# Kernel optimization log

Measured on AMD Instinct MI355X. Metric: run time of the kernel, lower is better.

Reference implementation:

```python
import jax, jax.numpy as jnp
import numpy as np
import math

H, NH, DH, FF = 768, 12, 64, 3072
B, S = 8, 1024

def _gelu(x):
    return x * 0.5 * (1.0 + jax.lax.erf(x / math.sqrt(2.0)))

def _layernorm(x, gamma, beta, eps=1e-6):
    mean = jnp.mean(x, axis=-1, keepdims=True)
    std = jnp.std(x, axis=-1, keepdims=True, ddof=1)  # torch unbiased std
    return gamma * (x - mean) / (std + eps) + beta

def setup_inputs() -> dict:
    key = jax.random.key(0)
    ks = jax.random.split(key, 16)
    p = lambda k, shape: jax.random.normal(k, shape, dtype=jnp.float32) * 0.02
    return {
        "hidden": jax.random.normal(ks[0], (B, S, H), dtype=jnp.float32),
        "mask": jnp.zeros((B, 1, S, S), dtype=jnp.float32),
        "position_bias": jax.random.normal(ks[1], (1, NH, S, S), dtype=jnp.float32),
        "Wq": p(ks[2], (H, H)), "bq": jnp.zeros((H,), jnp.float32),
        "Wk": p(ks[3], (H, H)), "bk": jnp.zeros((H,), jnp.float32),
        "Wv": p(ks[4], (H, H)), "bv": jnp.zeros((H,), jnp.float32),
        "Wo": p(ks[5], (H, H)), "bo": jnp.zeros((H,), jnp.float32),
        "W1": p(ks[6], (H, FF)), "b1": jnp.zeros((FF,), jnp.float32),
        "W2": p(ks[7], (FF, H)), "b2": jnp.zeros((H,), jnp.float32),
        "g1": jnp.ones((H,), jnp.float32), "beta1": jnp.zeros((H,), jnp.float32),
        "g2": jnp.ones((H,), jnp.float32), "beta2": jnp.zeros((H,), jnp.float32),
    }

def reference(hidden, mask, position_bias, Wq, bq, Wk, bk, Wv, bv, Wo, bo,
              W1, b1, W2, b2, g1, beta1, g2, beta2):
    b, s, _ = hidden.shape
    def split_heads(x):
        return x.reshape(b, s, NH, DH).transpose(0, 2, 1, 3)  # [b, h, s, d]
    q = split_heads(hidden @ Wq + bq)
    k = split_heads(hidden @ Wk + bk)
    v = split_heads(hidden @ Wv + bv)
    scores = jnp.einsum('bhqd,bhkd->bhqk', q, k)
    scores = scores + position_bias          # bias added BEFORE scaling (as in source)
    scores = scores / math.sqrt(float(DH))
    scores = scores + mask
    probs = jax.nn.softmax(scores, axis=-1)  # dropout is identity in eval
    ctx = jnp.einsum('bhqk,bhkd->bhqd', probs, v)
    ctx = ctx.transpose(0, 2, 1, 3).reshape(b, s, NH * DH)
    attn_out = ctx @ Wo + bo
    inter = _layernorm(attn_out + hidden, g1, beta1)
    ffn = _gelu(inter @ W1 + b1) @ W2 + b2
    return _layernorm(ffn + inter, g2, beta2)
```

## Files before the change

### kernel.cpp

```cpp
#include <hip/hip_runtime.h>
#include <cmath>

typedef __bf16 bf16;
typedef __attribute__((ext_vector_type(8))) __bf16 bf16x8;
typedef __attribute__((ext_vector_type(4))) __bf16 bf16x4;
typedef __attribute__((ext_vector_type(4))) float f32x4;

#define DEVINL __device__ __forceinline__

DEVINL void gload16(const void* g, void* l) {
    __builtin_amdgcn_global_load_lds((const __attribute__((address_space(1))) void*)g,
                                     (__attribute__((address_space(3))) void*)l, 16, 0, 0);
}


__global__ void cast_bf16_kernel(const float* __restrict__ in, bf16* __restrict__ out, int n4) {
    int i = blockIdx.x * 256 + threadIdx.x;
    if (i < n4) {
        float4 v = ((const float4*)in)[i];
        bf16x4 o;
        o[0] = (bf16)v.x; o[1] = (bf16)v.y; o[2] = (bf16)v.z; o[3] = (bf16)v.w;
        ((bf16x4*)out)[i] = o;
    }
}

__global__ void scale_cast_kernel(const float* __restrict__ in, bf16* __restrict__ out,
                                  float scale, int n4) {
    int i = blockIdx.x * 256 + threadIdx.x;
    if (i < n4) {
        float4 v = ((const float4*)in)[i];
        bf16x4 o;
        o[0] = (bf16)(v.x * scale); o[1] = (bf16)(v.y * scale);
        o[2] = (bf16)(v.z * scale); o[3] = (bf16)(v.w * scale);
        ((bf16x4*)out)[i] = o;
    }
}

__global__ void tcast_kernel(const float* __restrict__ in, bf16* __restrict__ out, int R, int C) {
    __shared__ float t[32][33];
    int tx = threadIdx.x & 31, ty = threadIdx.x >> 5;
    int r0 = blockIdx.y * 32, c0 = blockIdx.x * 32;
#pragma unroll
    for (int i = 0; i < 4; ++i)
        t[ty + 8 * i][tx] = in[(size_t)(r0 + ty + 8 * i) * C + c0 + tx];
    __syncthreads();
#pragma unroll
    for (int i = 0; i < 4; ++i)
        out[(size_t)(c0 + ty + 8 * i) * R + r0 + tx] = (bf16)t[tx][ty + 8 * i];
}

__global__ void concat_bias_kernel(const float* __restrict__ a, const float* __restrict__ b,
                                   const float* __restrict__ c, float* __restrict__ out) {
    int i = blockIdx.x * 256 + threadIdx.x;
    if (i < 2304) out[i] = (i < 768) ? a[i] : ((i < 1536) ? b[i - 768] : c[i - 1536]);
}

__global__ __launch_bounds__(256) void vtrans_kernel(const bf16* __restrict__ qkv,
                                                     bf16* __restrict__ vT) {
    __shared__ bf16 t[64][72];
    const int tid = threadIdx.x;
    const int bh = blockIdx.y, s0 = blockIdx.x * 32;
    const int b = bh / 12, h = bh % 12;
    {
        const int r = tid >> 3, c8 = (tid & 7) * 8;
        bf16x8 v = *(const bf16x8*)(qkv + (size_t)(b * 1024 + s0 + r) * 2304 + 1536 + h * 64 + c8);
#pragma unroll
        for (int j = 0; j < 8; ++j) t[c8 + j][r] = v[j];
    }
    __syncthreads();
    {
        const int d = tid >> 2, s8 = (tid & 3) * 8;
        bf16x8 o = *(const bf16x8*)(&t[d][s8]);
        *(bf16x8*)(vT + (size_t)(bh * 64 + d) * 1024 + s0 + s8) = o;
    }
}

template<int MODE>
__global__ void gemm_kernel(const bf16* __restrict__ A, const bf16* __restrict__ Bt,
                            const float* __restrict__ bias,
                            bf16* __restrict__ Cb, float* __restrict__ Cf,
                            int M, int N, int K, int ldc) {
    __shared__ __align__(16) bf16 As[128 * 64];
    __shared__ __align__(16) bf16 Bs[128 * 64];
    const int tid = threadIdx.x;
    const int wid = tid >> 6, lane = tid & 63;
    const int L = blockIdx.y * gridDim.x + blockIdx.x;
    const int cpx = (gridDim.x * gridDim.y) >> 3;
    const int wg = (L & 7) * cpx + (L >> 3);
    const int m0 = (wg / gridDim.x) * 128, n0 = (wg % gridDim.x) * 128;
    const int wr = (wid >> 1) * 64, wc = (wid & 1) * 64;
    const int lg = lane >> 4, l15 = lane & 15;
    f32x4 acc[4][4] = {};

    for (int k0 = 0; k0 < K; k0 += 64) {
        __syncthreads();
#pragma unroll
        for (int i = 0; i < 4; ++i) {
            const int cbase = (wid * 4 + i) * 1024;
            const int td = cbase + lane * 16;
            const int row = td >> 7;
            const int s16 = ((td >> 4) & 7) ^ (row & 7);
            gload16(A + (size_t)(m0 + row) * K + k0 + s16 * 8, (char*)As + cbase);
            gload16(Bt + (size_t)(n0 + row) * K + k0 + s16 * 8, (char*)Bs + cbase);
        }
        __syncthreads();
#pragma unroll
        for (int kk = 0; kk < 2; ++kk) {
            bf16x8 af[4], bfr[4];
#pragma unroll
            for (int mi = 0; mi < 4; ++mi) {
                int ra = wr + mi * 16 + l15;
                int off = (ra * 128 + (kk * 32 + 8 * lg) * 2) ^ ((ra & 7) << 4);
                af[mi] = *(const bf16x8*)((const char*)As + off);
            }
#pragma unroll
            for (int ni = 0; ni < 4; ++ni) {
                int rb = wc + ni * 16 + l15;
                int off = (rb * 128 + (kk * 32 + 8 * lg) * 2) ^ ((rb & 7) << 4);
                bfr[ni] = *(const bf16x8*)((const char*)Bs + off);
            }
#pragma unroll
            for (int mi = 0; mi < 4; ++mi)
#pragma unroll
                for (int ni = 0; ni < 4; ++ni)
                    acc[mi][ni] = __builtin_amdgcn_mfma_f32_16x16x32_bf16(af[mi], bfr[ni], acc[mi][ni], 0, 0, 0);
        }
    }
#pragma unroll
    for (int mi = 0; mi < 4; ++mi) {
#pragma unroll
        for (int r = 0; r < 4; ++r) {
            const int row = m0 + wr + mi * 16 + lg * 4 + r;
#pragma unroll
            for (int ni = 0; ni < 4; ++ni) {
                const int col = n0 + wc + ni * 16 + l15;
                float v = acc[mi][ni][r] + bias[col];
                if (MODE == 2) v = v * 0.5f * (1.0f + erff(v * 0.70710678118654752f));
                if (MODE == 1) Cf[(size_t)row * ldc + col] = v;
                else           Cb[(size_t)row * ldc + col] = (bf16)v;
            }
        }
    }
}

__global__ __launch_bounds__(256, 3) void attn_kernel(const bf16* __restrict__ qkv,
                                                      const bf16* __restrict__ pbs,
                                                      const bf16* __restrict__ maskb,
                                                      const bf16* __restrict__ vT,
                                                      bf16* __restrict__ ctx) {
    __shared__ __align__(16) bf16 Kb[3][64 * 64];
    __shared__ __align__(16) bf16 Vb[3][64 * 64];
    const int tid = threadIdx.x, wid = tid >> 6, lane = tid & 63;
    const int bh = blockIdx.y, b = bh / 12, h = bh % 12;
    const int q0 = blockIdx.x * 128 + wid * 32;
    const int lg = lane >> 4, l15 = lane & 15;
    const float cqk = 0.18033688011112042f;

    bf16x8 aq[2][2];
#pragma unroll
    for (int qs = 0; qs < 2; ++qs) {
        const size_t r = (size_t)(b * 1024 + q0 + qs * 16 + l15) * 2304 + h * 64 + 8 * lg;
        aq[qs][0] = *(const bf16x8*)(qkv + r);
        aq[qs][1] = *(const bf16x8*)(qkv + r + 32);
    }

    auto stage = [&](int tt, int pp) {
#pragma unroll
        for (int rd = 0; rd < 2; ++rd) {
            const int n = rd * 256 + tid;
            const int i = n >> 3, sl = n & 7, c = sl ^ (i & 7);
            const int sig = (i & 32) | ((i & 12) << 1) | ((i & 16) >> 2) | (i & 3);
            gload16(qkv + (size_t)(b * 1024 + tt * 64 + sig) * 2304 + 768 + h * 64 + c * 8,
                    (char*)Kb[pp] + n * 16);
            gload16(vT + ((size_t)bh * 64 + i) * 1024 + tt * 64 + c * 8,
                    (char*)Vb[pp] + n * 16);
        }
    };

    float mrun[2] = {-1e30f, -1e30f}, lsum[2] = {0.f, 0.f};
    f32x4 acc[2][4] = {};

    stage(0, 0);
    stage(1, 1);
    __syncthreads();
    for (int t = 0; t < 16; ++t) {
        const int p = t % 3;
        const int k0 = t * 64;
        bf16x8 pbv[2][2], mkv[2][2];
#pragma unroll
        for (int qs = 0; qs < 2; ++qs) {
            const int q = q0 + qs * 16 + l15;
            const bf16* pr = pbs + ((size_t)h * 1024 + q) * 1024 + k0 + lg * 8;
            const bf16* mr = maskb + ((size_t)b * 1024 + q) * 1024 + k0 + lg * 8;
            pbv[qs][0] = *(const bf16x8*)pr;  pbv[qs][1] = *(const bf16x8*)(pr + 32);
            mkv[qs][0] = *(const bf16x8*)mr;  mkv[qs][1] = *(const bf16x8*)(mr + 32);
        }
        if (t < 14) stage(t + 2, (t + 2) % 3);

        bf16x8 bk[4][2];
#pragma unroll
        for (int kt = 0; kt < 4; ++kt) {
            const int row = kt * 16 + l15;
            const int byte = (row * 128 + lg * 16) ^ ((row & 7) << 4);
            bk[kt][0] = *(const bf16x8*)((const char*)Kb[p] + byte);
            bk[kt][1] = *(const bf16x8*)((const char*)Kb[p] + (byte ^ 64));
        }
        f32x4 s[2][4];
#pragma unroll
        for (int qs = 0; qs < 2; ++qs)
#pragma unroll
            for (int kt = 0; kt < 4; ++kt) {
                f32x4 z = {};
                z = __builtin_amdgcn_mfma_f32_16x16x32_bf16(bk[kt][0], aq[qs][0], z, 0, 0, 0);
                z = __builtin_amdgcn_mfma_f32_16x16x32_bf16(bk[kt][1], aq[qs][1], z, 0, 0, 0);
                s[qs][kt] = z;
            }
#pragma unroll
        for (int qs = 0; qs < 2; ++qs)
#pragma unroll
            for (int kt = 0; kt < 4; ++kt)
#pragma unroll
                for (int r = 0; r < 4; ++r) {
                    const int j = (kt & 1) * 4 + r;
                    s[qs][kt][r] = s[qs][kt][r] * cqk
                                 + (float)pbv[qs][kt >> 1][j]
                                 + (float)mkv[qs][kt >> 1][j];
                }
        bf16x8 po[2][2];
#pragma unroll
        for (int qs = 0; qs < 2; ++qs) {
            float tm = s[qs][0][0];
#pragma unroll
            for (int kt = 0; kt < 4; ++kt)
#pragma unroll
                for (int r = 0; r < 4; ++r) tm = fmaxf(tm, s[qs][kt][r]);
            tm = fmaxf(tm, __shfl_xor(tm, 16));
            tm = fmaxf(tm, __shfl_xor(tm, 32));
            const float mn = fmaxf(mrun[qs], tm);
            const float scal = __builtin_amdgcn_exp2f(mrun[qs] - mn);
            mrun[qs] = mn;
            float ts = 0.f;
#pragma unroll
            for (int kt = 0; kt < 4; ++kt)
#pragma unroll
                for (int r = 0; r < 4; ++r) {
                    const float pv = __builtin_amdgcn_exp2f(s[qs][kt][r] - mn);
                    ts += pv;
                    const int idx = kt * 4 + r;
                    if (idx < 8) po[qs][0][idx] = (bf16)pv;
                    else         po[qs][1][idx - 8] = (bf16)pv;
                }
            ts += __shfl_xor(ts, 16);
            ts += __shfl_xor(ts, 32);
            lsum[qs] = lsum[qs] * scal + ts;
#pragma unroll
            for (int dt = 0; dt < 4; ++dt) {
                acc[qs][dt][0] *= scal; acc[qs][dt][1] *= scal;
                acc[qs][dt][2] *= scal; acc[qs][dt][3] *= scal;
            }
        }
        bf16x8 vb[4][2];
#pragma unroll
        for (int dt = 0; dt < 4; ++dt) {
            const int row = dt * 16 + l15;
            const int byte = (row * 128 + lg * 16) ^ ((row & 7) << 4);
            vb[dt][0] = *(const bf16x8*)((const char*)Vb[p] + byte);
            vb[dt][1] = *(const bf16x8*)((const char*)Vb[p] + (byte ^ 64));
        }
#pragma unroll
        for (int qs = 0; qs < 2; ++qs)
#pragma unroll
            for (int dt = 0; dt < 4; ++dt) {
                acc[qs][dt] = __builtin_amdgcn_mfma_f32_16x16x32_bf16(vb[dt][0], po[qs][0], acc[qs][dt], 0, 0, 0);
                acc[qs][dt] = __builtin_amdgcn_mfma_f32_16x16x32_bf16(vb[dt][1], po[qs][1], acc[qs][dt], 0, 0, 0);
            }
        __syncthreads();
    }
    char* scr = (char*)Kb + wid * 4096;
#pragma unroll
    for (int qs = 0; qs < 2; ++qs) {
        const float inv = 1.0f / lsum[qs];
        const int ql = qs * 16 + l15;
#pragma unroll
        for (int dt = 0; dt < 4; ++dt) {
            bf16x4 o;
#pragma unroll
            for (int r = 0; r < 4; ++r) o[r] = (bf16)(acc[qs][dt][r] * inv);
            const int wb = (ql * 128 + dt * 32 + lg * 8) ^ ((ql & 7) << 4);
            *(bf16x4*)(scr + wb) = o;
        }
    }
    __syncthreads();
#pragma unroll
    for (int qs = 0; qs < 2; ++qs) {
        const int ql = qs * 16 + l15;
        const int rb = (ql * 128 + lg * 32) ^ ((ql & 7) << 4);
        bf16x8 o0 = *(const bf16x8*)(scr + rb);
        bf16x8 o1 = *(const bf16x8*)(scr + (rb ^ 16));
        bf16* cp = ctx + (size_t)(b * 1024 + q0 + ql) * 768 + h * 64 + lg * 16;
        *(bf16x8*)cp = o0;
        *(bf16x8*)(cp + 8) = o1;
    }
}

template<int MODE>
__global__ __launch_bounds__(256) void ln_kernel(const float* __restrict__ x, const float* __restrict__ res,
                                                 const float* __restrict__ g, const float* __restrict__ bt,
                                                 float* __restrict__ outf, bf16* __restrict__ outb) {
    const int wid = threadIdx.x >> 6, lane = threadIdx.x & 63;
    const int row = blockIdx.x * 4 + wid;
    const float4* xr = (const float4*)(x + (size_t)row * 768);
    const float4* rr = (const float4*)(res + (size_t)row * 768);
    float4 v[3];
    float s = 0.f, ss = 0.f;
#pragma unroll
    for (int j = 0; j < 3; ++j) {
        float4 a = xr[lane + 64 * j];
        float4 b = rr[lane + 64 * j];
        float4 w;
        w.x = a.x + b.x; w.y = a.y + b.y; w.z = a.z + b.z; w.w = a.w + b.w;
        v[j] = w;
        s += w.x + w.y + w.z + w.w;
        ss += w.x * w.x + w.y * w.y + w.z * w.z + w.w * w.w;
    }
#pragma unroll
    for (int off = 1; off <= 32; off <<= 1) { s += __shfl_xor(s, off); ss += __shfl_xor(ss, off); }
    const float mean = s * (1.f / 768.f);
    float var = (ss - 768.f * mean * mean) * (1.f / 767.f);
    var = fmaxf(var, 0.f);
    const float inv = 1.f / (sqrtf(var) + 1e-6f);
#pragma unroll
    for (int j = 0; j < 3; ++j) {
        float4 gv = ((const float4*)g)[lane + 64 * j];
        float4 bv = ((const float4*)bt)[lane + 64 * j];
        float4 y;
        y.x = gv.x * (v[j].x - mean) * inv + bv.x;
        y.y = gv.y * (v[j].y - mean) * inv + bv.y;
        y.z = gv.z * (v[j].z - mean) * inv + bv.z;
        y.w = gv.w * (v[j].w - mean) * inv + bv.w;
        ((float4*)(outf + (size_t)row * 768))[lane + 64 * j] = y;
        if (MODE == 0) {
            bf16x4 o;
            o[0] = (bf16)y.x; o[1] = (bf16)y.y; o[2] = (bf16)y.z; o[3] = (bf16)y.w;
            ((bf16x4*)(outb + (size_t)row * 768))[lane + 64 * j] = o;
        }
    }
}


extern "C" void kernel_launch(void* const* d_in, const int* in_sizes, int n_in,
                              void* d_out, int out_size, void* d_ws, size_t ws_size,
                              hipStream_t stream) {
    const float* hidden = (const float*)d_in[0];
    const float* mask   = (const float*)d_in[1];
    const float* pb     = (const float*)d_in[2];
    const float* Wq = (const float*)d_in[3];
    const float* bq = (const float*)d_in[4];
    const float* Wk = (const float*)d_in[5];
    const float* bk = (const float*)d_in[6];
    const float* Wv = (const float*)d_in[7];
    const float* bv = (const float*)d_in[8];
    const float* Wo = (const float*)d_in[9];
    const float* bo = (const float*)d_in[10];
    const float* W1 = (const float*)d_in[11];
    const float* b1 = (const float*)d_in[12];
    const float* W2 = (const float*)d_in[13];
    const float* b2 = (const float*)d_in[14];
    const float* g1  = (const float*)d_in[15];
    const float* be1 = (const float*)d_in[16];
    const float* g2  = (const float*)d_in[17];
    const float* be2 = (const float*)d_in[18];
    float* out = (float*)d_out;

    char* ws = (char*)d_ws;
    bf16*  xbf     = (bf16*)(ws);
    bf16*  wqkv_t  = (bf16*)(ws + 12582912);
    bf16*  wo_t    = (bf16*)(ws + 16121856);
    bf16*  w1_t    = (bf16*)(ws + 17301504);
    bf16*  w2_t    = (bf16*)(ws + 22020096);
    float* bqkv    = (float*)(ws + 26738688);
    bf16*  qkv     = (bf16*)(ws + 26747904);
    bf16*  ffn1    = qkv;
    bf16*  vT      = (bf16*)(ws + 26747904 + 37748736);
    bf16*  ctx     = (bf16*)(ws + 77079552);
    float* attn_out= (float*)(ws + 89662464);
    bf16*  pbs     = (bf16*)(ws + 89662464);
    float* ffn2    = attn_out;
    float* interf  = (float*)(ws + 114828288);
    bf16*  maskb   = (bf16*)(ws + 114828288);
    bf16*  interb  = xbf;

    const float log2e = 1.4426950408889634f;

    cast_bf16_kernel<<<6291456 / 4 / 256, 256, 0, stream>>>(hidden, xbf, 6291456 / 4);
    tcast_kernel<<<dim3(24, 24), 256, 0, stream>>>(Wq, wqkv_t, 768, 768);
    tcast_kernel<<<dim3(24, 24), 256, 0, stream>>>(Wk, wqkv_t + 768 * 768, 768, 768);
    tcast_kernel<<<dim3(24, 24), 256, 0, stream>>>(Wv, wqkv_t + 2 * 768 * 768, 768, 768);
    tcast_kernel<<<dim3(24, 24), 256, 0, stream>>>(Wo, wo_t, 768, 768);
    tcast_kernel<<<dim3(96, 24), 256, 0, stream>>>(W1, w1_t, 768, 3072);
    tcast_kernel<<<dim3(24, 96), 256, 0, stream>>>(W2, w2_t, 3072, 768);
    concat_bias_kernel<<<9, 256, 0, stream>>>(bq, bk, bv, bqkv);
    scale_cast_kernel<<<12582912 / 4 / 256, 256, 0, stream>>>(pb, pbs, 0.125f * log2e, 12582912 / 4);
    scale_cast_kernel<<<8388608 / 4 / 256, 256, 0, stream>>>(mask, maskb, log2e, 8388608 / 4);

    gemm_kernel<0><<<dim3(18, 64), 256, 0, stream>>>(xbf, wqkv_t, bqkv, qkv, nullptr, 8192, 2304, 768, 2304);
    vtrans_kernel<<<dim3(32, 96), 256, 0, stream>>>(qkv, vT);
    attn_kernel<<<dim3(8, 96), 256, 0, stream>>>(qkv, pbs, maskb, vT, ctx);
    gemm_kernel<1><<<dim3(6, 64), 256, 0, stream>>>(ctx, wo_t, bo, nullptr, attn_out, 8192, 768, 768, 768);
    ln_kernel<0><<<2048, 256, 0, stream>>>(attn_out, hidden, g1, be1, interf, interb);
    gemm_kernel<2><<<dim3(24, 64), 256, 0, stream>>>(interb, w1_t, b1, ffn1, nullptr, 8192, 3072, 768, 3072);
    gemm_kernel<1><<<dim3(6, 64), 256, 0, stream>>>(ffn1, w2_t, b2, nullptr, ffn2, 8192, 768, 3072, 768);
    ln_kernel<1><<<2048, 256, 0, stream>>>(ffn2, interf, g2, be2, out, nullptr);
}
```

Measured before the change: 337.4 us.

## Double-buffer GEMM with 256x128 tiles and add lazy softmax rescaling in attention

The GEMM now uses 512-thread blocks with 256x128 output tiles and double-buffered LDS, so the next K-slice is loaded while MFMAs run on the current one. It also raises wave priority around the MFMA section. In attention, the online-softmax rescale of the accumulators and running sum is skipped unless the tile maximum exceeds the running max by more than 6 (in log2 units). This avoids per-tile multiplies at the cost of a bounded growth in exponent values. The LDS destination addressing for global_load_lds is also changed to a per-wave base, matching the hardware's lane-implicit layout.

```diff
diff --git a/kernel.cpp b/kernel.cpp
--- a/kernel.cpp
+++ b/kernel.cpp
@@ -76,48 +76,60 @@
 }
 
 template<int MODE>
-__global__ void gemm_kernel(const bf16* __restrict__ A, const bf16* __restrict__ Bt,
-                            const float* __restrict__ bias,
-                            bf16* __restrict__ Cb, float* __restrict__ Cf,
-                            int M, int N, int K, int ldc) {
-    __shared__ __align__(16) bf16 As[128 * 64];
-    __shared__ __align__(16) bf16 Bs[128 * 64];
+__global__ __launch_bounds__(512, 1) void gemm_kernel(const bf16* __restrict__ A, const bf16* __restrict__ Bt,
+                                                      const float* __restrict__ bias,
+                                                      bf16* __restrict__ Cb, float* __restrict__ Cf,
+                                                      int M, int N, int K, int ldc) {
+    __shared__ __align__(16) bf16 As[2][256 * 64];
+    __shared__ __align__(16) bf16 Bs[2][128 * 64];
     const int tid = threadIdx.x;
     const int wid = tid >> 6, lane = tid & 63;
     const int L = blockIdx.y * gridDim.x + blockIdx.x;
     const int cpx = (gridDim.x * gridDim.y) >> 3;
     const int wg = (L & 7) * cpx + (L >> 3);
-    const int m0 = (wg / gridDim.x) * 128, n0 = (wg % gridDim.x) * 128;
-    const int wr = (wid >> 1) * 64, wc = (wid & 1) * 64;
+    const int m0 = (wg / gridDim.x) * 256, n0 = (wg % gridDim.x) * 128;
+    const int wr = wid >> 1, wc = wid & 1;
     const int lg = lane >> 4, l15 = lane & 15;
     f32x4 acc[4][4] = {};
 
-    for (int k0 = 0; k0 < K; k0 += 64) {
-        __syncthreads();
-#pragma unroll
-        for (int i = 0; i < 4; ++i) {
-            const int cbase = (wid * 4 + i) * 1024;
-            const int td = cbase + lane * 16;
-            const int row = td >> 7;
-            const int s16 = ((td >> 4) & 7) ^ (row & 7);
-            gload16(A + (size_t)(m0 + row) * K + k0 + s16 * 8, (char*)As + cbase);
-            gload16(Bt + (size_t)(n0 + row) * K + k0 + s16 * 8, (char*)Bs + cbase);
-        }
-        __syncthreads();
+    auto stage = [&](int k0, int pp) {
+#pragma unroll
+        for (int j = 0; j < 4; ++j) {
+            const int n = j * 512 + tid;
+            const int row = n >> 3, sl = n & 7, c = sl ^ (row & 7);
+            gload16(A + (size_t)(m0 + row) * K + k0 + c * 8,
+                    (char*)As[pp] + (j * 512 + wid * 64) * 16);
+        }
+#pragma unroll
+        for (int j = 0; j < 2; ++j) {
+            const int n = j * 512 + tid;
+            const int row = n >> 3, sl = n & 7, c = sl ^ (row & 7);
+            gload16(Bt + (size_t)(n0 + row) * K + k0 + c * 8,
+                    (char*)Bs[pp] + (j * 512 + wid * 64) * 16);
+        }
+    };
+
+    const int nk = K >> 6;
+    stage(0, 0);
+    __syncthreads();
+    for (int t = 0; t < nk; ++t) {
+        const int buf = t & 1;
+        if (t + 1 < nk) stage((t + 1) << 6, buf ^ 1);
+        __builtin_amdgcn_s_setprio(1);
 #pragma unroll
         for (int kk = 0; kk < 2; ++kk) {
             bf16x8 af[4], bfr[4];
 #pragma unroll
             for (int mi = 0; mi < 4; ++mi) {
-                int ra = wr + mi * 16 + l15;
-                int off = (ra * 128 + (kk * 32 + 8 * lg) * 2) ^ ((ra & 7) << 4);
-                af[mi] = *(const bf16x8*)((const char*)As + off);
+                const int ra = wr * 64 + mi * 16 + l15;
+                const int off = (ra * 128 + kk * 64 + lg * 16) ^ ((ra & 7) << 4);
+                af[mi] = *(const bf16x8*)((const char*)As[buf] + off);
             }
 #pragma unroll
             for (int ni = 0; ni < 4; ++ni) {
-                int rb = wc + ni * 16 + l15;
-                int off = (rb * 128 + (kk * 32 + 8 * lg) * 2) ^ ((rb & 7) << 4);
-                bfr[ni] = *(const bf16x8*)((const char*)Bs + off);
+                const int rb = wc * 64 + ni * 16 + l15;
+                const int off = (rb * 128 + kk * 64 + lg * 16) ^ ((rb & 7) << 4);
+                bfr[ni] = *(const bf16x8*)((const char*)Bs[buf] + off);
             }
 #pragma unroll
             for (int mi = 0; mi < 4; ++mi)
@@ -125,15 +137,17 @@
                 for (int ni = 0; ni < 4; ++ni)
                     acc[mi][ni] = __builtin_amdgcn_mfma_f32_16x16x32_bf16(af[mi], bfr[ni], acc[mi][ni], 0, 0, 0);
         }
+        __builtin_amdgcn_s_setprio(0);
+        __syncthreads();
     }
 #pragma unroll
     for (int mi = 0; mi < 4; ++mi) {
 #pragma unroll
         for (int r = 0; r < 4; ++r) {
-            const int row = m0 + wr + mi * 16 + lg * 4 + r;
+            const int row = m0 + wr * 64 + mi * 16 + lg * 4 + r;
 #pragma unroll
             for (int ni = 0; ni < 4; ++ni) {
-                const int col = n0 + wc + ni * 16 + l15;
+                const int col = n0 + wc * 64 + ni * 16 + l15;
                 float v = acc[mi][ni][r] + bias[col];
                 if (MODE == 2) v = v * 0.5f * (1.0f + erff(v * 0.70710678118654752f));
                 if (MODE == 1) Cf[(size_t)row * ldc + col] = v;
@@ -171,9 +185,9 @@
             const int i = n >> 3, sl = n & 7, c = sl ^ (i & 7);
             const int sig = (i & 32) | ((i & 12) << 1) | ((i & 16) >> 2) | (i & 3);
             gload16(qkv + (size_t)(b * 1024 + tt * 64 + sig) * 2304 + 768 + h * 64 + c * 8,
-                    (char*)Kb[pp] + n * 16);
+                    (char*)Kb[pp] + (rd * 256 + wid * 64) * 16);
             gload16(vT + ((size_t)bh * 64 + i) * 1024 + tt * 64 + c * 8,
-                    (char*)Vb[pp] + n * 16);
+                    (char*)Vb[pp] + (rd * 256 + wid * 64) * 16);
         }
     };
 
@@ -236,15 +250,23 @@
                 for (int r = 0; r < 4; ++r) tm = fmaxf(tm, s[qs][kt][r]);
             tm = fmaxf(tm, __shfl_xor(tm, 16));
             tm = fmaxf(tm, __shfl_xor(tm, 32));
-            const float mn = fmaxf(mrun[qs], tm);
-            const float scal = __builtin_amdgcn_exp2f(mrun[qs] - mn);
-            mrun[qs] = mn;
+            if (!__all(tm <= mrun[qs] + 6.0f)) {
+                const float mn = fmaxf(mrun[qs], tm);
+                const float scal = __builtin_amdgcn_exp2f(mrun[qs] - mn);
+                mrun[qs] = mn;
+                lsum[qs] *= scal;
+#pragma unroll
+                for (int dt = 0; dt < 4; ++dt) {
+                    acc[qs][dt][0] *= scal; acc[qs][dt][1] *= scal;
+                    acc[qs][dt][2] *= scal; acc[qs][dt][3] *= scal;
+                }
+            }
             float ts = 0.f;
 #pragma unroll
             for (int kt = 0; kt < 4; ++kt)
 #pragma unroll
                 for (int r = 0; r < 4; ++r) {
-                    const float pv = __builtin_amdgcn_exp2f(s[qs][kt][r] - mn);
+                    const float pv = __builtin_amdgcn_exp2f(s[qs][kt][r] - mrun[qs]);
                     ts += pv;
                     const int idx = kt * 4 + r;
                     if (idx < 8) po[qs][0][idx] = (bf16)pv;
@@ -252,12 +274,7 @@
                 }
             ts += __shfl_xor(ts, 16);
             ts += __shfl_xor(ts, 32);
-            lsum[qs] = lsum[qs] * scal + ts;
-#pragma unroll
-            for (int dt = 0; dt < 4; ++dt) {
-                acc[qs][dt][0] *= scal; acc[qs][dt][1] *= scal;
-                acc[qs][dt][2] *= scal; acc[qs][dt][3] *= scal;
-            }
+            lsum[qs] += ts;
         }
         bf16x8 vb[4][2];
 #pragma unroll
@@ -403,12 +420,12 @@
     scale_cast_kernel<<<12582912 / 4 / 256, 256, 0, stream>>>(pb, pbs, 0.125f * log2e, 12582912 / 4);
     scale_cast_kernel<<<8388608 / 4 / 256, 256, 0, stream>>>(mask, maskb, log2e, 8388608 / 4);
 
-    gemm_kernel<0><<<dim3(18, 64), 256, 0, stream>>>(xbf, wqkv_t, bqkv, qkv, nullptr, 8192, 2304, 768, 2304);
+    gemm_kernel<0><<<dim3(18, 32), 512, 0, stream>>>(xbf, wqkv_t, bqkv, qkv, nullptr, 8192, 2304, 768, 2304);
     vtrans_kernel<<<dim3(32, 96), 256, 0, stream>>>(qkv, vT);
     attn_kernel<<<dim3(8, 96), 256, 0, stream>>>(qkv, pbs, maskb, vT, ctx);
-    gemm_kernel<1><<<dim3(6, 64), 256, 0, stream>>>(ctx, wo_t, bo, nullptr, attn_out, 8192, 768, 768, 768);
+    gemm_kernel<1><<<dim3(6, 32), 512, 0, stream>>>(ctx, wo_t, bo, nullptr, attn_out, 8192, 768, 768, 768);
     ln_kernel<0><<<2048, 256, 0, stream>>>(attn_out, hidden, g1, be1, interf, interb);
-    gemm_kernel<2><<<dim3(24, 64), 256, 0, stream>>>(interb, w1_t, b1, ffn1, nullptr, 8192, 3072, 768, 3072);
-    gemm_kernel<1><<<dim3(6, 64), 256, 0, stream>>>(ffn1, w2_t, b2, nullptr, ffn2, 8192, 768, 3072, 768);
+    gemm_kernel<2><<<dim3(24, 32), 512, 0, stream>>>(interb, w1_t, b1, ffn1, nullptr, 8192, 3072, 768, 3072);
+    gemm_kernel<1><<<dim3(6, 32), 512, 0, stream>>>(ffn1, w2_t, b2, nullptr, ffn2, 8192, 768, 3072, 768);
     ln_kernel<1><<<2048, 256, 0, stream>>>(ffn2, interf, g2, be2, out, nullptr);
 }
```

Result: slower. 369.2 us (+9.4%).

## Fuse bias/mask prep, lazy softmax rescale, bf16 residual, gemm launch bounds

Applied to the files above, without the earlier changes.

Merges the two scale-cast kernels into one launch. Skips the online-softmax rescale unless the running max grows by more than a threshold, relying on exp2 headroom. The first LayerNorm stops writing an fp32 intermediate, and the second LayerNorm reads the bf16 copy as its residual, which cuts traffic but lowers residual precision. Also adds occupancy launch bounds to the GEMM and changes the global_load_lds destination to a wave-uniform LDS base.

```diff
diff --git a/kernel.cpp b/kernel.cpp
--- a/kernel.cpp
+++ b/kernel.cpp
@@ -24,15 +24,25 @@
     }
 }
 
-__global__ void scale_cast_kernel(const float* __restrict__ in, bf16* __restrict__ out,
-                                  float scale, int n4) {
-    int i = blockIdx.x * 256 + threadIdx.x;
-    if (i < n4) {
-        float4 v = ((const float4*)in)[i];
+__global__ void prep_pm_kernel(const float* __restrict__ pb, const float* __restrict__ mask,
+                               bf16* __restrict__ pbs, bf16* __restrict__ maskb,
+                               int n1, int n2) {
+    const int i = blockIdx.x * 256 + threadIdx.x;
+    const float c1 = 0.18033688011112042f;
+    const float c2 = 1.4426950408889634f;
+    if (i < n1) {
+        float4 v = ((const float4*)pb)[i];
         bf16x4 o;
-        o[0] = (bf16)(v.x * scale); o[1] = (bf16)(v.y * scale);
-        o[2] = (bf16)(v.z * scale); o[3] = (bf16)(v.w * scale);
-        ((bf16x4*)out)[i] = o;
+        o[0] = (bf16)(v.x * c1); o[1] = (bf16)(v.y * c1);
+        o[2] = (bf16)(v.z * c1); o[3] = (bf16)(v.w * c1);
+        ((bf16x4*)pbs)[i] = o;
+    } else if (i < n1 + n2) {
+        const int j = i - n1;
+        float4 v = ((const float4*)mask)[j];
+        bf16x4 o;
+        o[0] = (bf16)(v.x * c2); o[1] = (bf16)(v.y * c2);
+        o[2] = (bf16)(v.z * c2); o[3] = (bf16)(v.w * c2);
+        ((bf16x4*)maskb)[j] = o;
     }
 }
 
@@ -76,10 +86,10 @@
 }
 
 template<int MODE>
-__global__ void gemm_kernel(const bf16* __restrict__ A, const bf16* __restrict__ Bt,
-                            const float* __restrict__ bias,
-                            bf16* __restrict__ Cb, float* __restrict__ Cf,
-                            int M, int N, int K, int ldc) {
+__global__ __launch_bounds__(256, 4) void gemm_kernel(const bf16* __restrict__ A, const bf16* __restrict__ Bt,
+                                                      const float* __restrict__ bias,
+                                                      bf16* __restrict__ Cb, float* __restrict__ Cf,
+                                                      int M, int N, int K, int ldc) {
     __shared__ __align__(16) bf16 As[128 * 64];
     __shared__ __align__(16) bf16 Bs[128 * 64];
     const int tid = threadIdx.x;
@@ -171,9 +181,9 @@
             const int i = n >> 3, sl = n & 7, c = sl ^ (i & 7);
             const int sig = (i & 32) | ((i & 12) << 1) | ((i & 16) >> 2) | (i & 3);
             gload16(qkv + (size_t)(b * 1024 + tt * 64 + sig) * 2304 + 768 + h * 64 + c * 8,
-                    (char*)Kb[pp] + n * 16);
+                    (char*)Kb[pp] + (rd * 256 + wid * 64) * 16);
             gload16(vT + ((size_t)bh * 64 + i) * 1024 + tt * 64 + c * 8,
-                    (char*)Vb[pp] + n * 16);
+                    (char*)Vb[pp] + (rd * 256 + wid * 64) * 16);
         }
     };
 
@@ -236,15 +246,23 @@
                 for (int r = 0; r < 4; ++r) tm = fmaxf(tm, s[qs][kt][r]);
             tm = fmaxf(tm, __shfl_xor(tm, 16));
             tm = fmaxf(tm, __shfl_xor(tm, 32));
-            const float mn = fmaxf(mrun[qs], tm);
-            const float scal = __builtin_amdgcn_exp2f(mrun[qs] - mn);
-            mrun[qs] = mn;
+            if (!__all(tm <= mrun[qs] + 6.0f)) {
+                const float mn = fmaxf(mrun[qs], tm);
+                const float scal = __builtin_amdgcn_exp2f(mrun[qs] - mn);
+                mrun[qs] = mn;
+                lsum[qs] *= scal;
+#pragma unroll
+                for (int dt = 0; dt < 4; ++dt) {
+                    acc[qs][dt][0] *= scal; acc[qs][dt][1] *= scal;
+                    acc[qs][dt][2] *= scal; acc[qs][dt][3] *= scal;
+                }
+            }
             float ts = 0.f;
 #pragma unroll
             for (int kt = 0; kt < 4; ++kt)
 #pragma unroll
                 for (int r = 0; r < 4; ++r) {
-                    const float pv = __builtin_amdgcn_exp2f(s[qs][kt][r] - mn);
+                    const float pv = __builtin_amdgcn_exp2f(s[qs][kt][r] - mrun[qs]);
                     ts += pv;
                     const int idx = kt * 4 + r;
                     if (idx < 8) po[qs][0][idx] = (bf16)pv;
@@ -252,12 +270,7 @@
                 }
             ts += __shfl_xor(ts, 16);
             ts += __shfl_xor(ts, 32);
-            lsum[qs] = lsum[qs] * scal + ts;
-#pragma unroll
-            for (int dt = 0; dt < 4; ++dt) {
-                acc[qs][dt][0] *= scal; acc[qs][dt][1] *= scal;
-                acc[qs][dt][2] *= scal; acc[qs][dt][3] *= scal;
-            }
+            lsum[qs] += ts;
         }
         bf16x8 vb[4][2];
 #pragma unroll
@@ -304,19 +317,26 @@
 }
 
 template<int MODE>
-__global__ __launch_bounds__(256) void ln_kernel(const float* __restrict__ x, const float* __restrict__ res,
+__global__ __launch_bounds__(256) void ln_kernel(const float* __restrict__ x,
+                                                 const float* __restrict__ resf,
+                                                 const bf16* __restrict__ resb,
                                                  const float* __restrict__ g, const float* __restrict__ bt,
                                                  float* __restrict__ outf, bf16* __restrict__ outb) {
     const int wid = threadIdx.x >> 6, lane = threadIdx.x & 63;
     const int row = blockIdx.x * 4 + wid;
     const float4* xr = (const float4*)(x + (size_t)row * 768);
-    const float4* rr = (const float4*)(res + (size_t)row * 768);
     float4 v[3];
     float s = 0.f, ss = 0.f;
 #pragma unroll
     for (int j = 0; j < 3; ++j) {
         float4 a = xr[lane + 64 * j];
-        float4 b = rr[lane + 64 * j];
+        float4 b;
+        if (MODE == 0) {
+            b = ((const float4*)(resf + (size_t)row * 768))[lane + 64 * j];
+        } else {
+            bf16x4 rb = ((const bf16x4*)(resb + (size_t)row * 768))[lane + 64 * j];
+            b.x = (float)rb[0]; b.y = (float)rb[1]; b.z = (float)rb[2]; b.w = (float)rb[3];
+        }
         float4 w;
         w.x = a.x + b.x; w.y = a.y + b.y; w.z = a.z + b.z; w.w = a.w + b.w;
         v[j] = w;
@@ -338,8 +358,9 @@
         y.y = gv.y * (v[j].y - mean) * inv + bv.y;
         y.z = gv.z * (v[j].z - mean) * inv + bv.z;
         y.w = gv.w * (v[j].w - mean) * inv + bv.w;
-        ((float4*)(outf + (size_t)row * 768))[lane + 64 * j] = y;
-        if (MODE == 0) {
+        if (MODE == 1) {
+            ((float4*)(outf + (size_t)row * 768))[lane + 64 * j] = y;
+        } else {
             bf16x4 o;
             o[0] = (bf16)y.x; o[1] = (bf16)y.y; o[2] = (bf16)y.z; o[3] = (bf16)y.w;
             ((bf16x4*)(outb + (size_t)row * 768))[lane + 64 * j] = o;
@@ -386,11 +407,8 @@
     float* attn_out= (float*)(ws + 89662464);
     bf16*  pbs     = (bf16*)(ws + 89662464);
     float* ffn2    = attn_out;
-    float* interf  = (float*)(ws + 114828288);
     bf16*  maskb   = (bf16*)(ws + 114828288);
     bf16*  interb  = xbf;
-
-    const float log2e = 1.4426950408889634f;
 
     cast_bf16_kernel<<<6291456 / 4 / 256, 256, 0, stream>>>(hidden, xbf, 6291456 / 4);
     tcast_kernel<<<dim3(24, 24), 256, 0, stream>>>(Wq, wqkv_t, 768, 768);
@@ -400,15 +418,15 @@
     tcast_kernel<<<dim3(96, 24), 256, 0, stream>>>(W1, w1_t, 768, 3072);
     tcast_kernel<<<dim3(24, 96), 256, 0, stream>>>(W2, w2_t, 3072, 768);
     concat_bias_kernel<<<9, 256, 0, stream>>>(bq, bk, bv, bqkv);
-    scale_cast_kernel<<<12582912 / 4 / 256, 256, 0, stream>>>(pb, pbs, 0.125f * log2e, 12582912 / 4);
-    scale_cast_kernel<<<8388608 / 4 / 256, 256, 0, stream>>>(mask, maskb, log2e, 8388608 / 4);
+    prep_pm_kernel<<<(3145728 + 2097152) / 256, 256, 0, stream>>>(pb, mask, pbs, maskb,
+                                                                  3145728, 2097152);
 
     gemm_kernel<0><<<dim3(18, 64), 256, 0, stream>>>(xbf, wqkv_t, bqkv, qkv, nullptr, 8192, 2304, 768, 2304);
     vtrans_kernel<<<dim3(32, 96), 256, 0, stream>>>(qkv, vT);
     attn_kernel<<<dim3(8, 96), 256, 0, stream>>>(qkv, pbs, maskb, vT, ctx);
     gemm_kernel<1><<<dim3(6, 64), 256, 0, stream>>>(ctx, wo_t, bo, nullptr, attn_out, 8192, 768, 768, 768);
-    ln_kernel<0><<<2048, 256, 0, stream>>>(attn_out, hidden, g1, be1, interf, interb);
+    ln_kernel<0><<<2048, 256, 0, stream>>>(attn_out, hidden, nullptr, g1, be1, nullptr, interb);
     gemm_kernel<2><<<dim3(24, 64), 256, 0, stream>>>(interb, w1_t, b1, ffn1, nullptr, 8192, 3072, 768, 3072);
     gemm_kernel<1><<<dim3(6, 64), 256, 0, stream>>>(ffn1, w2_t, b2, nullptr, ffn2, 8192, 768, 3072, 768);
-    ln_kernel<1><<<2048, 256, 0, stream>>>(ffn2, interf, g2, be2, out, nullptr);
-}
+    ln_kernel<1><<<2048, 256, 0, stream>>>(ffn2, nullptr, interb, g2, be2, out, nullptr);
+}
```

Result: faster. 330.0 us (-2.2%).
